# Performance work log

Measured on AMD Instinct MI355X. Metric: run time of the kernel, lower is better.

The kernel has to match this reference:

```python
import jax, jax.numpy as jnp
import numpy as np

DIM = 1024
HEADS = 16
HEAD_DIM = DIM // HEADS
EPS = 1e-6


def setup_inputs() -> dict:
    key = jax.random.key(0)
    ks = jax.random.split(key, 4)
    x = jax.random.normal(ks[0], (2, 2048, DIM), dtype=jnp.float32)
    W_qkv = jax.random.normal(ks[1], (3 * DIM, DIM), dtype=jnp.float32) * (DIM ** -0.5)
    q_gamma = jnp.ones((HEAD_DIM,), jnp.float32)
    q_beta = jnp.zeros((HEAD_DIM,), jnp.float32)
    k_gamma = jnp.ones((HEAD_DIM,), jnp.float32)
    k_beta = jnp.zeros((HEAD_DIM,), jnp.float32)
    W_proj = jax.random.normal(ks[2], (DIM, DIM), dtype=jnp.float32) * (DIM ** -0.5)
    b_proj = jnp.zeros((DIM,), jnp.float32)
    return {"x": x, "W_qkv": W_qkv, "q_gamma": q_gamma, "q_beta": q_beta,
            "k_gamma": k_gamma, "k_beta": k_beta, "W_proj": W_proj, "b_proj": b_proj}


def _layernorm(x, gamma, beta):
    mu = jnp.mean(x, axis=-1, keepdims=True)
    var = jnp.mean(jnp.square(x - mu), axis=-1, keepdims=True)
    return (x - mu) * jax.lax.rsqrt(var + EPS) * gamma + beta


def reference(x, W_qkv, q_gamma, q_beta, k_gamma, k_beta, W_proj, b_proj):
    B, N, C = x.shape
    H, D = HEADS, HEAD_DIM
    scale = D ** -0.5
    qkv = jnp.einsum('bnc,oc->bno', x, W_qkv)            # [B,N,3C]
    qkv = qkv.reshape(B, N, 3, H, D).transpose(2, 0, 3, 1, 4)  # [3,B,H,N,D]
    q, k, v = qkv[0], qkv[1], qkv[2]
    q = _layernorm(q, q_gamma, q_beta)
    k = _layernorm(k, k_gamma, k_beta)
    attn = jnp.einsum('bhnd,bhmd->bhnm', q * scale, k)   # [B,H,N,N]
    attn = jax.nn.softmax(attn, axis=-1)
    out = jnp.einsum('bhnm,bhmd->bhnd', attn, v)         # [B,H,N,D]
    out = out.transpose(0, 2, 1, 3).reshape(B, N, C)
    return jnp.einsum('bnc,oc->bno', out, W_proj) + b_proj
```

## Files before the change

### kernel.cpp

```cpp
#include <hip/hip_runtime.h>

#define DIM 1024
#define HEADS 16
#define HD 64
#define BATCH 2
#define SEQ 2048
#define ROWS (BATCH*SEQ)
#define EPS 1e-6f

typedef float f32x4  __attribute__((ext_vector_type(4)));
typedef float f32x16 __attribute__((ext_vector_type(16)));
typedef short s16x4  __attribute__((ext_vector_type(4)));
typedef short s16x8  __attribute__((ext_vector_type(8)));

static __device__ __forceinline__ short f2bf(float f) {
    union { float f; unsigned u; } x; x.f = f;
    unsigned r = x.u + 0x7FFFu + ((x.u >> 16) & 1u);
    return (short)(r >> 16);
}
static __device__ __forceinline__ s16x8 pack8(float4 lo, float4 hi) {
    s16x8 r;
    r[0]=f2bf(lo.x); r[1]=f2bf(lo.y); r[2]=f2bf(lo.z); r[3]=f2bf(lo.w);
    r[4]=f2bf(hi.x); r[5]=f2bf(hi.y); r[6]=f2bf(hi.z); r[7]=f2bf(hi.w);
    return r;
}
static __device__ __forceinline__ unsigned cvtpk(float a, float b) {
    unsigned r;
    asm("v_cvt_pk_bf16_f32 %0, %1, %2" : "=v"(r) : "v"(a), "v"(b));
    return r;
}
static __device__ __forceinline__ void gld16(short* l, const short* g) {
    __builtin_amdgcn_global_load_lds(
        (const __attribute__((address_space(1))) void*)g,
        (__attribute__((address_space(3))) void*)l, 16, 0, 0);
}

#define MFMA32(A,B,C) __builtin_amdgcn_mfma_f32_32x32x16_bf16(A, B, C, 0, 0, 0)
#define MFMA16(A,B,C) __builtin_amdgcn_mfma_f32_16x16x32_bf16(A, B, C, 0, 0, 0)

__global__ __launch_bounds__(256) void convert3(
    const float* __restrict__ x, const float* __restrict__ wq,
    const float* __restrict__ wp,
    short* __restrict__ xb, short* __restrict__ wqb, short* __restrict__ wpb)
{
    const int idx = blockIdx.x * 256 + threadIdx.x;
    const int C1 = 4194304/8, C2 = 3145728/8;
    const float* src; short* dst; int off;
    if (idx < C1)            { src = x;  dst = xb;  off = idx; }
    else if (idx < C1 + C2)  { src = wq; dst = wqb; off = idx - C1; }
    else                     { src = wp; dst = wpb; off = idx - C1 - C2; }
    float4 a = ((const float4*)src)[off*2];
    float4 b = ((const float4*)src)[off*2 + 1];
    ((s16x8*)dst)[off] = pack8(a, b);
}

#define BKG 64

template<int MODE>
__global__ __launch_bounds__(256) void gemm_bf16(
    const short* __restrict__ A, const short* __restrict__ W,
    const float* __restrict__ bias,
    const float* __restrict__ qg, const float* __restrict__ qbeta,
    const float* __restrict__ kg, const float* __restrict__ kbeta,
    short* __restrict__ qb, short* __restrict__ kb, short* __restrict__ vb,
    float* __restrict__ out)
{
    alignas(16) __shared__ short As[128*BKG];
    alignas(16) __shared__ short Bs[128*BKG];
    const int tid  = threadIdx.x;
    const int lane = tid & 63, wave = tid >> 6;
    const int wr = wave >> 1, wc = wave & 1;
    const int c = lane & 15, g = lane >> 4;
    const int brow = blockIdx.y * 128, bcol = blockIdx.x * 128;

    const int srow = lane >> 3;
    const int scol = (lane & 7) * 8;
    const short* ag = A + (size_t)(brow + srow)*DIM + scol;
    const short* wg = W + (size_t)(bcol + srow)*DIM + scol;

    f32x4 acc[4][4] = {};

    for (int k0 = 0; k0 < DIM; k0 += BKG) {
        #pragma unroll
        for (int j = 0; j < 4; j++) {
            const int rg = (wave*4 + j) * 8;
            gld16(&As[rg*BKG], ag + (size_t)rg*DIM + k0);
            gld16(&Bs[rg*BKG], wg + (size_t)rg*DIM + k0);
        }
        __syncthreads();

        #pragma unroll
        for (int ks = 0; ks < 2; ks++) {
            s16x8 af[4], bf[4];
            #pragma unroll
            for (int m = 0; m < 4; m++)
                af[m] = *(const s16x8*)&As[(wr*64 + m*16 + c)*BKG + ks*32 + g*8];
            #pragma unroll
            for (int n = 0; n < 4; n++)
                bf[n] = *(const s16x8*)&Bs[(wc*64 + n*16 + c)*BKG + ks*32 + g*8];
            #pragma unroll
            for (int m = 0; m < 4; m++)
                #pragma unroll
                for (int n = 0; n < 4; n++)
                    acc[m][n] = MFMA16(af[m], bf[n], acc[m][n]);
        }
        __syncthreads();
    }

    if (MODE == 0) {
        const int colbase = bcol + wc*64;
        const int t = colbase >> 10;
        const int h = (colbase >> 6) & 15;
        short* dst = (t == 0) ? qb : (t == 1) ? kb : vb;
        float gam[4], bet[4];
        float scale = 1.0f;
        if (t < 2) {
            const float* G  = (t == 0) ? qg : kg;
            const float* Bt = (t == 0) ? qbeta : kbeta;
            #pragma unroll
            for (int n = 0; n < 4; n++) { gam[n] = G[n*16 + c]; bet[n] = Bt[n*16 + c]; }
            if (t == 0) scale = 0.125f * 1.44269504088896340736f;
        }
        #pragma unroll
        for (int m = 0; m < 4; m++) {
            #pragma unroll
            for (int j = 0; j < 4; j++) {
                const int row = brow + wr*64 + m*16 + g*4 + j;
                const int bi = row >> 11, ni = row & (SEQ-1);
                const size_t rb = ((size_t)(bi*HEADS + h)*SEQ + ni)*HD;
                float v0 = acc[m][0][j], v1 = acc[m][1][j];
                float v2 = acc[m][2][j], v3 = acc[m][3][j];
                if (t < 2) {
                    float s = (v0 + v1) + (v2 + v3);
                    s += __shfl_xor(s, 1); s += __shfl_xor(s, 2);
                    s += __shfl_xor(s, 4); s += __shfl_xor(s, 8);
                    const float mu = s * 0.015625f;
                    v0 -= mu; v1 -= mu; v2 -= mu; v3 -= mu;
                    float vv = (v0*v0 + v1*v1) + (v2*v2 + v3*v3);
                    vv += __shfl_xor(vv, 1); vv += __shfl_xor(vv, 2);
                    vv += __shfl_xor(vv, 4); vv += __shfl_xor(vv, 8);
                    const float rstd = rsqrtf(vv * 0.015625f + EPS);
                    v0 = (v0*rstd*gam[0] + bet[0]) * scale;
                    v1 = (v1*rstd*gam[1] + bet[1]) * scale;
                    v2 = (v2*rstd*gam[2] + bet[2]) * scale;
                    v3 = (v3*rstd*gam[3] + bet[3]) * scale;
                }
                dst[rb + 0*16 + c] = f2bf(v0);
                dst[rb + 1*16 + c] = f2bf(v1);
                dst[rb + 2*16 + c] = f2bf(v2);
                dst[rb + 3*16 + c] = f2bf(v3);
            }
        }
    } else {
        #pragma unroll
        for (int n = 0; n < 4; n++) {
            const int col = bcol + wc*64 + n*16 + c;
            const float bv = bias[col];
            #pragma unroll
            for (int m = 0; m < 4; m++) {
                #pragma unroll
                for (int j = 0; j < 4; j++) {
                    const int row = brow + wr*64 + m*16 + g*4 + j;
                    out[(size_t)row*DIM + col] = acc[m][n][j] + bv;
                }
            }
        }
    }
}

__global__ __launch_bounds__(256) void repack_kv(
    const short* __restrict__ kin, const short* __restrict__ vin,
    short* __restrict__ KP, short* __restrict__ VP)
{
    constexpr int LT = 72;
    alignas(16) __shared__ short Kl[64*LT];
    alignas(16) __shared__ short Vl[64*LT];
    const int bh = blockIdx.x, n0 = blockIdx.y * 64;
    const int tid = threadIdx.x;
    const int r = tid >> 2, cq = (tid & 3) * 16;
    {
        const short* ksrc = kin + ((size_t)bh*SEQ + n0 + r)*HD + cq;
        const short* vsrc = vin + ((size_t)bh*SEQ + n0 + r)*HD + cq;
        *(s16x8*)&Kl[r*LT + cq]     = *(const s16x8*)ksrc;
        *(s16x8*)&Kl[r*LT + cq + 8] = *(const s16x8*)(ksrc + 8);
        *(s16x8*)&Vl[r*LT + cq]     = *(const s16x8*)vsrc;
        *(s16x8*)&Vl[r*LT + cq + 8] = *(const s16x8*)(vsrc + 8);
    }
    __syncthreads();
    const int tt = tid >> 7;
    const int r2 = tid & 127;
    const int sub = r2 >> 5, lp = r2 & 31;
    const size_t tbase = ((size_t)bh*64 + blockIdx.y*2 + tt)*2048 + sub*512;
    #pragma unroll
    for (int g2 = 0; g2 < 2; g2++) {
        const int lane = 2*lp + g2;
        s16x8 val = *(const s16x8*)&Kl[(tt*32 + (lane & 31))*LT + sub*16 + 8*(lane >> 5)];
        *(s16x8*)&KP[tbase + lane*8] = val;
    }
    #pragma unroll
    for (int g2 = 0; g2 < 2; g2++) {
        const int lane = 2*lp + g2;
        const int hi = lane >> 5, l31 = lane & 31;
        s16x8 val;
        #pragma unroll
        for (int e = 0; e < 8; e++)
            val[e] = Vl[(tt*32 + (sub >> 1)*16 + 8*hi + e)*LT + (sub & 1)*32 + l31];
        *(s16x8*)&VP[tbase + lane*8] = val;
    }
}

__global__ __launch_bounds__(256) void attn_kernel(
    const short* __restrict__ qbuf, const short* __restrict__ KP,
    const short* __restrict__ VP, short* __restrict__ aout)
{
    alignas(16) __shared__ float OL[2][64][32];
    __shared__ float ML[2][2][64];

    const int bh = blockIdx.x, qt = blockIdx.y;
    const int tid = threadIdx.x, wave = tid >> 6, lane = tid & 63;
    const int qsub = wave >> 1, half = wave & 1;
    const int l31 = lane & 31, hi = lane >> 5;
    const int q0 = qt*64 + qsub*32;

    s16x8 qf[4];
    const short* qrow = qbuf + ((size_t)bh*SEQ + q0 + l31)*HD + 8*hi;
    #pragma unroll
    for (int ks = 0; ks < 4; ks++) qf[ks] = *(const s16x8*)(qrow + 16*ks);

    const short* kp = KP + ((size_t)bh*64 + half*32)*2048 + lane*8;
    const short* vp = VP + ((size_t)bh*64 + half*32)*2048 + lane*8;

    f32x16 o0 = {}, o1 = {};
    float m = -1e30f, l = 0.f;

    for (int it = 0; it < 32; it++) {
        s16x8 kc0 = *(const s16x8*)(kp);
        s16x8 kc1 = *(const s16x8*)(kp + 512);
        s16x8 kc2 = *(const s16x8*)(kp + 1024);
        s16x8 kc3 = *(const s16x8*)(kp + 1536);
        s16x8 vc0 = *(const s16x8*)(vp);
        s16x8 vc1 = *(const s16x8*)(vp + 512);
        s16x8 vc2 = *(const s16x8*)(vp + 1024);
        s16x8 vc3 = *(const s16x8*)(vp + 1536);
        kp += 2048; vp += 2048;
        __builtin_amdgcn_sched_barrier(0);

        f32x16 s = {};
        __builtin_amdgcn_s_setprio(1);
        s = MFMA32(kc0, qf[0], s);
        s = MFMA32(kc1, qf[1], s);
        s = MFMA32(kc2, qf[2], s);
        s = MFMA32(kc3, qf[3], s);
        __builtin_amdgcn_s_setprio(0);

        float t8[8];
        #pragma unroll
        for (int i = 0; i < 8; i++) t8[i] = fmaxf(s[i], s[i+8]);
        #pragma unroll
        for (int i = 0; i < 4; i++) t8[i] = fmaxf(t8[i], t8[i+4]);
        float pmax = fmaxf(fmaxf(t8[0], t8[2]), fmaxf(t8[1], t8[3]));
        pmax = fmaxf(pmax, __shfl_xor(pmax, 32));

        if (!__all(pmax - m <= 8.0f)) {
            float mn = fmaxf(m, pmax);
            float corr = exp2f(m - mn);
            #pragma unroll
            for (int i = 0; i < 16; i++) { o0[i] *= corr; o1[i] *= corr; }
            l *= corr;
            m = mn;
        }
        #pragma unroll
        for (int i = 0; i < 16; i++) s[i] = exp2f(s[i] - m);
        float a8[8];
        #pragma unroll
        for (int i = 0; i < 8; i++) a8[i] = s[i] + s[i+8];
        #pragma unroll
        for (int i = 0; i < 4; i++) a8[i] += a8[i+4];
        float rs = (a8[0] + a8[2]) + (a8[1] + a8[3]);
        rs += __shfl_xor(rs, 32);
        l += rs;

        s16x8 pa0, pa1;
        {
            unsigned A0 = cvtpk(s[0], s[1]),  A1 = cvtpk(s[2], s[3]);
            unsigned B0 = cvtpk(s[4], s[5]),  B1 = cvtpk(s[6], s[7]);
            asm volatile("v_permlane32_swap_b32 %0, %1" : "+v"(A0), "+v"(B0));
            asm volatile("v_permlane32_swap_b32 %0, %1" : "+v"(A1), "+v"(B1));
            union { s16x8 v; unsigned u[4]; } w;
            w.u[0]=A0; w.u[1]=A1; w.u[2]=B0; w.u[3]=B1;
            pa0 = w.v;
            unsigned C0 = cvtpk(s[8], s[9]),  C1 = cvtpk(s[10], s[11]);
            unsigned D0 = cvtpk(s[12], s[13]),D1 = cvtpk(s[14], s[15]);
            asm volatile("v_permlane32_swap_b32 %0, %1" : "+v"(C0), "+v"(D0));
            asm volatile("v_permlane32_swap_b32 %0, %1" : "+v"(C1), "+v"(D1));
            union { s16x8 v; unsigned u[4]; } w2;
            w2.u[0]=C0; w2.u[1]=C1; w2.u[2]=D0; w2.u[3]=D1;
            pa1 = w2.v;
        }

        __builtin_amdgcn_s_setprio(1);
        o0 = MFMA32(vc0, pa0, o0);
        o1 = MFMA32(vc1, pa0, o1);
        o0 = MFMA32(vc2, pa1, o0);
        o1 = MFMA32(vc3, pa1, o1);
        __builtin_amdgcn_s_setprio(0);
    }

    if (half == 1) {
        float* ob = &OL[qsub][lane][0];
        #pragma unroll
        for (int i = 0; i < 8; i++) {
            const int slot = (i + (lane & 7)) & 7;
            f32x4 v;
            if (i < 4) { v[0]=o0[4*i]; v[1]=o0[4*i+1]; v[2]=o0[4*i+2]; v[3]=o0[4*i+3]; }
            else { const int j = i-4; v[0]=o1[4*j]; v[1]=o1[4*j+1]; v[2]=o1[4*j+2]; v[3]=o1[4*j+3]; }
            *(f32x4*)(ob + slot*4) = v;
        }
        ML[qsub][0][lane] = m;
        ML[qsub][1][lane] = l;
    }
    __syncthreads();
    if (half == 0) {
        const float m1 = ML[qsub][0][lane];
        const float l1 = ML[qsub][1][lane];
        const float ms = fmaxf(m, m1);
        const float c0 = exp2f(m - ms), c1 = exp2f(m1 - ms);
        const float inv = 1.0f / (l*c0 + l1*c1);
        const float* ob = &OL[qsub][lane][0];
        const int b = bh >> 4, h = bh & 15;
        short* dst = aout + ((size_t)(b*SEQ + q0 + l31))*DIM + h*HD;
        #pragma unroll
        for (int i = 0; i < 8; i++) {
            const int slot = (i + (lane & 7)) & 7;
            f32x4 p = *(const f32x4*)(ob + slot*4);
            s16x4 st;
            if (i < 4) {
                #pragma unroll
                for (int j = 0; j < 4; j++) st[j] = f2bf((o0[4*i+j]*c0 + p[j]*c1) * inv);
                *(s16x4*)(dst + 8*i + 4*hi) = st;
            } else {
                const int t3 = i - 4;
                #pragma unroll
                for (int j = 0; j < 4; j++) st[j] = f2bf((o1[4*t3+j]*c0 + p[j]*c1) * inv);
                *(s16x4*)(dst + 32 + 8*t3 + 4*hi) = st;
            }
        }
    }
}

extern "C" void kernel_launch(void* const* d_in, const int* in_sizes, int n_in,
                              void* d_out, int out_size, void* d_ws, size_t ws_size,
                              hipStream_t stream)
{
    const float* x     = (const float*)d_in[0];
    const float* Wqkv  = (const float*)d_in[1];
    const float* qg    = (const float*)d_in[2];
    const float* qbeta = (const float*)d_in[3];
    const float* kg    = (const float*)d_in[4];
    const float* kbeta = (const float*)d_in[5];
    const float* Wproj = (const float*)d_in[6];
    const float* bproj = (const float*)d_in[7];
    float* out = (float*)d_out;

    char* ws = (char*)d_ws;
    const size_t MB = 1024*1024;
    short* xb     = (short*)(ws);
    short* KP     = (short*)(ws);
    short* wqkvb  = (short*)(ws + 8*MB);
    short* wprojb = (short*)(ws + 14*MB);
    short* q      = (short*)(ws + 16*MB);
    short* k      = (short*)(ws + 24*MB);
    short* aout   = (short*)(ws + 24*MB);
    short* vrow   = (short*)(ws + 32*MB);
    short* VP     = (short*)(ws + 40*MB);

    convert3<<<dim3(4096), 256, 0, stream>>>(x, Wqkv, Wproj, xb, wqkvb, wprojb);

    gemm_bf16<0><<<dim3(3*DIM/128, ROWS/128), 256, 0, stream>>>(
        xb, wqkvb, nullptr, qg, qbeta, kg, kbeta, q, k, vrow, nullptr);

    repack_kv<<<dim3(BATCH*HEADS, SEQ/64), 256, 0, stream>>>(k, vrow, KP, VP);

    attn_kernel<<<dim3(BATCH*HEADS, SEQ/64), 256, 0, stream>>>(q, KP, VP, aout);

    gemm_bf16<1><<<dim3(DIM/128, ROWS/128), 256, 0, stream>>>(
        aout, wprojb, bproj, nullptr, nullptr, nullptr, nullptr,
        nullptr, nullptr, nullptr, out);
}
```

Measured before the change: 150.3 us.

## Software-pipeline attention loop: overlap next QK^T MFMA with current softmax

Restructures the attention inner loop so the QK^T MFMAs for tile t+1 are issued before the softmax of tile t, using ping-pong score registers (sA/sB) and a loop unrolled by two. K fragments are prefetched two tiles ahead and V fragments one tile ahead, so global loads no longer sit directly before their use. The aim is to hide MFMA latency and load latency behind the exp and reduction work. In exchange it raises register pressure, and on the last iterations it issues wrapped-around (redundant) loads and one extra QK^T MFMA group whose result is discarded.

New measurement: 148.1 us. About the same (-1.4%).

```diff
diff --git a/kernel.cpp b/kernel.cpp
--- a/kernel.cpp
+++ b/kernel.cpp
@@ -37,6 +37,42 @@
 
 #define MFMA32(A,B,C) __builtin_amdgcn_mfma_f32_32x32x16_bf16(A, B, C, 0, 0, 0)
 #define MFMA16(A,B,C) __builtin_amdgcn_mfma_f32_16x16x32_bf16(A, B, C, 0, 0, 0)
+
+struct PA { s16x8 a, b; };
+static __device__ __forceinline__ PA packP(const f32x16& s) {
+    PA r;
+    unsigned A0 = cvtpk(s[0], s[1]),  A1 = cvtpk(s[2], s[3]);
+    unsigned B0 = cvtpk(s[4], s[5]),  B1 = cvtpk(s[6], s[7]);
+    asm volatile("v_permlane32_swap_b32 %0, %1" : "+v"(A0), "+v"(B0));
+    asm volatile("v_permlane32_swap_b32 %0, %1" : "+v"(A1), "+v"(B1));
+    union { s16x8 v; unsigned u[4]; } w;
+    w.u[0]=A0; w.u[1]=A1; w.u[2]=B0; w.u[3]=B1;
+    r.a = w.v;
+    unsigned C0 = cvtpk(s[8], s[9]),   C1 = cvtpk(s[10], s[11]);
+    unsigned D0 = cvtpk(s[12], s[13]), D1 = cvtpk(s[14], s[15]);
+    asm volatile("v_permlane32_swap_b32 %0, %1" : "+v"(C0), "+v"(D0));
+    asm volatile("v_permlane32_swap_b32 %0, %1" : "+v"(C1), "+v"(D1));
+    union { s16x8 v; unsigned u[4]; } w2;
+    w2.u[0]=C0; w2.u[1]=C1; w2.u[2]=D0; w2.u[3]=D1;
+    r.b = w2.v;
+    return r;
+}
+static __device__ __forceinline__ float tree_max(const f32x16& s) {
+    float t[8];
+    #pragma unroll
+    for (int i = 0; i < 8; i++) t[i] = fmaxf(s[i], s[i+8]);
+    #pragma unroll
+    for (int i = 0; i < 4; i++) t[i] = fmaxf(t[i], t[i+4]);
+    return fmaxf(fmaxf(t[0], t[2]), fmaxf(t[1], t[3]));
+}
+static __device__ __forceinline__ float tree_sum(const f32x16& s) {
+    float t[8];
+    #pragma unroll
+    for (int i = 0; i < 8; i++) t[i] = s[i] + s[i+8];
+    #pragma unroll
+    for (int i = 0; i < 4; i++) t[i] += t[i+4];
+    return (t[0] + t[2]) + (t[1] + t[3]);
+}
 
 __global__ __launch_bounds__(256) void convert3(
     const float* __restrict__ x, const float* __restrict__ wq,
@@ -209,6 +245,59 @@
     }
 }
 
+#define ATTN_BODY(prev, nxt, t)                                              \
+    {                                                                        \
+                                  \
+        f32x16 zz_ = {};                                                     \
+        __builtin_amdgcn_s_setprio(1);                                       \
+        nxt = MFMA32(kc0, qf[0], zz_);                                       \
+        nxt = MFMA32(kc1, qf[1], nxt);                                       \
+        nxt = MFMA32(kc2, qf[2], nxt);                                       \
+        nxt = MFMA32(kc3, qf[3], nxt);                                       \
+        __builtin_amdgcn_s_setprio(0);                                       \
+                      \
+        {                                                                    \
+            const int nt2_ = (((t) + 2) & 31) * 2048;                        \
+            kc0 = *(const s16x8*)(kp + nt2_);                                \
+            kc1 = *(const s16x8*)(kp + nt2_ + 512);                          \
+            kc2 = *(const s16x8*)(kp + nt2_ + 1024);                         \
+            kc3 = *(const s16x8*)(kp + nt2_ + 1536);                         \
+        }                                                                    \
+        __builtin_amdgcn_sched_barrier(0);                                   \
+                            \
+        float pmax_ = tree_max(prev);                                        \
+        pmax_ = fmaxf(pmax_, __shfl_xor(pmax_, 32));                         \
+        if (!__all(pmax_ - m <= 8.0f)) {                                     \
+            float mn_ = fmaxf(m, pmax_);                                     \
+            float corr_ = exp2f(m - mn_);                                    \
+            _Pragma("unroll")                                                \
+            for (int i_ = 0; i_ < 16; i_++) { o0[i_] *= corr_; o1[i_] *= corr_; } \
+            l *= corr_;                                                      \
+            m = mn_;                                                         \
+        }                                                                    \
+        _Pragma("unroll")                                                    \
+        for (int i_ = 0; i_ < 16; i_++) prev[i_] = exp2f(prev[i_] - m);      \
+        float rs_ = tree_sum(prev);                                          \
+        rs_ += __shfl_xor(rs_, 32);                                          \
+        l += rs_;                                                            \
+        PA pa_ = packP(prev);                                                \
+                                        \
+        __builtin_amdgcn_s_setprio(1);                                       \
+        o0 = MFMA32(vc0, pa_.a, o0);                                         \
+        o1 = MFMA32(vc1, pa_.a, o1);                                         \
+        o0 = MFMA32(vc2, pa_.b, o0);                                         \
+        o1 = MFMA32(vc3, pa_.b, o1);                                         \
+        __builtin_amdgcn_s_setprio(0);                                       \
+                 \
+        {                                                                    \
+            const int nv_ = (((t) + 1) & 31) * 2048;                         \
+            vc0 = *(const s16x8*)(vp + nv_);                                 \
+            vc1 = *(const s16x8*)(vp + nv_ + 512);                           \
+            vc2 = *(const s16x8*)(vp + nv_ + 1024);                          \
+            vc3 = *(const s16x8*)(vp + nv_ + 1536);                          \
+        }                                                                    \
+    }
+
 __global__ __launch_bounds__(256) void attn_kernel(
     const short* __restrict__ qbuf, const short* __restrict__ KP,
     const short* __restrict__ VP, short* __restrict__ aout)
@@ -230,80 +319,37 @@
     const short* kp = KP + ((size_t)bh*64 + half*32)*2048 + lane*8;
     const short* vp = VP + ((size_t)bh*64 + half*32)*2048 + lane*8;
 
+    s16x8 kc0 = *(const s16x8*)(kp);
+    s16x8 kc1 = *(const s16x8*)(kp + 512);
+    s16x8 kc2 = *(const s16x8*)(kp + 1024);
+    s16x8 kc3 = *(const s16x8*)(kp + 1536);
+
     f32x16 o0 = {}, o1 = {};
     float m = -1e30f, l = 0.f;
 
-    for (int it = 0; it < 32; it++) {
-        s16x8 kc0 = *(const s16x8*)(kp);
-        s16x8 kc1 = *(const s16x8*)(kp + 512);
-        s16x8 kc2 = *(const s16x8*)(kp + 1024);
-        s16x8 kc3 = *(const s16x8*)(kp + 1536);
-        s16x8 vc0 = *(const s16x8*)(vp);
-        s16x8 vc1 = *(const s16x8*)(vp + 512);
-        s16x8 vc2 = *(const s16x8*)(vp + 1024);
-        s16x8 vc3 = *(const s16x8*)(vp + 1536);
-        kp += 2048; vp += 2048;
-        __builtin_amdgcn_sched_barrier(0);
-
-        f32x16 s = {};
+    f32x16 sA, sB;
+    {
+        f32x16 z = {};
         __builtin_amdgcn_s_setprio(1);
-        s = MFMA32(kc0, qf[0], s);
-        s = MFMA32(kc1, qf[1], s);
-        s = MFMA32(kc2, qf[2], s);
-        s = MFMA32(kc3, qf[3], s);
+        sA = MFMA32(kc0, qf[0], z);
+        sA = MFMA32(kc1, qf[1], sA);
+        sA = MFMA32(kc2, qf[2], sA);
+        sA = MFMA32(kc3, qf[3], sA);
         __builtin_amdgcn_s_setprio(0);
-
-        float t8[8];
-        #pragma unroll
-        for (int i = 0; i < 8; i++) t8[i] = fmaxf(s[i], s[i+8]);
-        #pragma unroll
-        for (int i = 0; i < 4; i++) t8[i] = fmaxf(t8[i], t8[i+4]);
-        float pmax = fmaxf(fmaxf(t8[0], t8[2]), fmaxf(t8[1], t8[3]));
-        pmax = fmaxf(pmax, __shfl_xor(pmax, 32));
-
-        if (!__all(pmax - m <= 8.0f)) {
-            float mn = fmaxf(m, pmax);
-            float corr = exp2f(m - mn);
-            #pragma unroll
-            for (int i = 0; i < 16; i++) { o0[i] *= corr; o1[i] *= corr; }
-            l *= corr;
-            m = mn;
-        }
-        #pragma unroll
-        for (int i = 0; i < 16; i++) s[i] = exp2f(s[i] - m);
-        float a8[8];
-        #pragma unroll
-        for (int i = 0; i < 8; i++) a8[i] = s[i] + s[i+8];
-        #pragma unroll
-        for (int i = 0; i < 4; i++) a8[i] += a8[i+4];
-        float rs = (a8[0] + a8[2]) + (a8[1] + a8[3]);
-        rs += __shfl_xor(rs, 32);
-        l += rs;
-
-        s16x8 pa0, pa1;
-        {
-            unsigned A0 = cvtpk(s[0], s[1]),  A1 = cvtpk(s[2], s[3]);
-            unsigned B0 = cvtpk(s[4], s[5]),  B1 = cvtpk(s[6], s[7]);
-            asm volatile("v_permlane32_swap_b32 %0, %1" : "+v"(A0), "+v"(B0));
-            asm volatile("v_permlane32_swap_b32 %0, %1" : "+v"(A1), "+v"(B1));
-            union { s16x8 v; unsigned u[4]; } w;
-            w.u[0]=A0; w.u[1]=A1; w.u[2]=B0; w.u[3]=B1;
-            pa0 = w.v;
-            unsigned C0 = cvtpk(s[8], s[9]),  C1 = cvtpk(s[10], s[11]);
-            unsigned D0 = cvtpk(s[12], s[13]),D1 = cvtpk(s[14], s[15]);
-            asm volatile("v_permlane32_swap_b32 %0, %1" : "+v"(C0), "+v"(D0));
-            asm volatile("v_permlane32_swap_b32 %0, %1" : "+v"(C1), "+v"(D1));
-            union { s16x8 v; unsigned u[4]; } w2;
-            w2.u[0]=C0; w2.u[1]=C1; w2.u[2]=D0; w2.u[3]=D1;
-            pa1 = w2.v;
-        }
-
-        __builtin_amdgcn_s_setprio(1);
-        o0 = MFMA32(vc0, pa0, o0);
-        o1 = MFMA32(vc1, pa0, o1);
-        o0 = MFMA32(vc2, pa1, o0);
-        o1 = MFMA32(vc3, pa1, o1);
-        __builtin_amdgcn_s_setprio(0);
+    }
+    kc0 = *(const s16x8*)(kp + 2048);
+    kc1 = *(const s16x8*)(kp + 2048 + 512);
+    kc2 = *(const s16x8*)(kp + 2048 + 1024);
+    kc3 = *(const s16x8*)(kp + 2048 + 1536);
+    s16x8 vc0 = *(const s16x8*)(vp);
+    s16x8 vc1 = *(const s16x8*)(vp + 512);
+    s16x8 vc2 = *(const s16x8*)(vp + 1024);
+    s16x8 vc3 = *(const s16x8*)(vp + 1536);
+
+    #pragma unroll 1
+    for (int it = 0; it < 32; it += 2) {
+        ATTN_BODY(sA, sB, it)
+        ATTN_BODY(sB, sA, it + 1)
     }
 
     if (half == 1) {
```
